# Optimization experiments

Measured on AMD Instinct MI355X. Metric: run time of the kernel, lower is better.

Reference implementation:

```python
import jax, jax.numpy as jnp
import numpy as np

B, N, DIM = 8, 1024, 768
HEADS = 8
NUM_CH = 3
S = 16  # sqrt(DIM // NUM_CH)
HEAD_DIM = DIM // HEADS
BN_EPS = 1e-3  # keras BatchNormalization default epsilon


def setup_inputs() -> dict:
    key = jax.random.key(0)
    ks = jax.random.split(key, 6)
    return {
        "q": jax.random.normal(ks[0], (B, N, DIM), jnp.float32),
        "k": jax.random.normal(ks[1], (B, N, DIM), jnp.float32),
        "v": jax.random.normal(ks[2], (B, N, DIM), jnp.float32),
        # qconv2d kernel (HWIO); source applies qconv2d to q, k AND v (kconv/vconv are dead)
        "conv_w": jax.random.normal(ks[3], (3, 3, NUM_CH, NUM_CH), jnp.float32) * 0.1,
        # re-attention 1x1 conv over the heads channel: (in_heads, out_heads) + bias
        "reatten_w": jax.random.normal(ks[4], (HEADS, HEADS), jnp.float32) * 0.3,
        "reatten_b": jnp.zeros((HEADS,), jnp.float32),
        # BatchNorm (inference) params over the heads channel
        "bn_gamma": jnp.ones((HEADS,), jnp.float32),
        "bn_beta": jnp.zeros((HEADS,), jnp.float32),
        "bn_mean": jnp.zeros((HEADS,), jnp.float32),
        "bn_var": jnp.ones((HEADS,), jnp.float32),
        "proj_w": jax.random.normal(ks[5], (DIM, DIM), jnp.float32) * 0.02,
        "proj_b": jnp.zeros((DIM,), jnp.float32),
    }


def _heads(x, conv_w):
    # x: (B, N, P) -> unflatten to (B*N, S, S, C) images, 3x3 SAME conv, split heads
    b, n, p = x.shape
    img = x.reshape(b * n, S, S, NUM_CH)
    y = jax.lax.conv_general_dilated(
        img, conv_w, window_strides=(1, 1), padding="SAME",
        dimension_numbers=("NHWC", "HWIO", "NHWC"))
    # (B, N, heads, head_dim) -> (B, heads, N, head_dim)
    return y.reshape(b, n, HEADS, p // HEADS).transpose(0, 2, 1, 3)


def reference(q, k, v, conv_w, reatten_w, reatten_b,
              bn_gamma, bn_beta, bn_mean, bn_var, proj_w, proj_b):
    scale = HEAD_DIM ** (-0.5)
    reatten_scale = 1.0  # transform_scale=False
    qh = _heads(q, conv_w)
    kh = _heads(k, conv_w)
    vh = _heads(v, conv_w)
    # (B, heads, N, N) attention map
    attn = jax.nn.softmax(jnp.einsum("bhnd,bhmd->bhnm", qh, kh) * scale, axis=-1)
    # re-attention: 1x1 conv mixing heads + inference BatchNorm over heads channel
    attn = jnp.einsum("bhnm,hg->bgnm", attn, reatten_w) + reatten_b[None, :, None, None]
    inv = bn_gamma * jax.lax.rsqrt(bn_var + BN_EPS)
    attn = (attn - bn_mean[None, :, None, None]) * inv[None, :, None, None] \
           + bn_beta[None, :, None, None]
    attn = attn * reatten_scale
    out = jnp.einsum("bhnm,bhmd->bhnd", attn, vh)  # (B, heads, N, head_dim)
    out = out.transpose(0, 2, 1, 3).reshape(q.shape[0], q.shape[1], DIM)
    return out @ proj_w + proj_b
```

## Files before the change

kernel.cpp:

```cpp
#include <hip/hip_runtime.h>
#include <hip/hip_bf16.h>
#include <stdint.h>

typedef __hip_bfloat16 bf16;
typedef __attribute__((ext_vector_type(8))) short short8;
typedef __attribute__((ext_vector_type(4))) float f32x4;

#define DEVFN __device__ __forceinline__

constexpr float SCALE = 0.10206207261596577f;

DEVFN short8 as_s8(uint4 u) { union { uint4 a; short8 b; } x; x.a = u; return x.b; }

DEVFN f32x4 mfma16(uint4 a, uint4 b, f32x4 c) {
  return __builtin_amdgcn_mfma_f32_16x16x32_bf16(as_s8(a), as_s8(b), c, 0, 0, 0);
}

DEVFN uint4 ldg4(const bf16* p) { return *(const uint4*)p; }

__global__ __launch_bounds__(256) void conv_kernel(
    const float* __restrict__ q, const float* __restrict__ k, const float* __restrict__ v,
    const float* __restrict__ cw,
    bf16* __restrict__ qh, bf16* __restrict__ kh, bf16* __restrict__ vh)
{
  __shared__ float img[3][768];
  __shared__ float wsm[81];
  const int t = threadIdx.x;
  const size_t pos = blockIdx.x;
  const int b = blockIdx.x >> 10;
  const int n = blockIdx.x & 1023;

  {
    const float* s0 = q + pos * 768;
    const float* s1 = k + pos * 768;
    const float* s2 = v + pos * 768;
    img[0][t] = s0[t]; img[0][t + 256] = s0[t + 256]; img[0][t + 512] = s0[t + 512];
    img[1][t] = s1[t]; img[1][t + 256] = s1[t + 256]; img[1][t + 512] = s1[t + 512];
    img[2][t] = s2[t]; img[2][t + 256] = s2[t + 256]; img[2][t + 512] = s2[t + 512];
  }
  if (t < 81) wsm[t] = cw[t];
  __syncthreads();

  const int x    = t & 15;
  const int y    = t >> 4;
  const int head = y >> 1;
  const int d0   = (y & 1) * 48 + x * 3;
  const size_t obase = (((size_t)(b * 8 + head)) * 1024 + n) * 96 + d0;

  #pragma unroll
  for (int s3 = 0; s3 < 3; ++s3) {
    float a0 = 0.f, a1 = 0.f, a2 = 0.f;
    #pragma unroll
    for (int dy = 0; dy < 3; ++dy) {
      const int iy = y + dy - 1;
      if ((unsigned)iy < 16u) {
        #pragma unroll
        for (int dx = 0; dx < 3; ++dx) {
          const int ix = x + dx - 1;
          if ((unsigned)ix < 16u) {
            const int ib = iy * 48 + ix * 3;
            const int wb = (dy * 3 + dx) * 9;
            #pragma unroll
            for (int ci = 0; ci < 3; ++ci) {
              const float val = img[s3][ib + ci];
              a0 = fmaf(val, wsm[wb + ci * 3 + 0], a0);
              a1 = fmaf(val, wsm[wb + ci * 3 + 1], a1);
              a2 = fmaf(val, wsm[wb + ci * 3 + 2], a2);
            }
          }
        }
      }
    }
    bf16* dst = (s3 == 0) ? qh : (s3 == 1) ? kh : vh;
    dst[obase]     = __float2bfloat16(a0);
    dst[obase + 1] = __float2bfloat16(a1);
    dst[obase + 2] = __float2bfloat16(a2);
  }
}

__global__ __launch_bounds__(256) void vtrans_kernel(
    const bf16* __restrict__ vh, bf16* __restrict__ vt)
{
  __shared__ unsigned T[64][52];
  const int t = threadIdx.x;
  const int bg = blockIdx.x >> 4;
  const int n0 = (blockIdx.x & 15) << 6;
  const bf16* src = vh + ((size_t)bg * 1024 + n0) * 96;
  #pragma unroll
  for (int it = 0; it < 3; ++it) {
    const int i = t + it * 256;
    const int r = i / 12, j = i - r * 12;
    ((uint4*)&T[r][0])[j] = ((const uint4*)(src + (size_t)r * 96))[j];
  }
  __syncthreads();
  #pragma unroll
  for (int it = 0; it < 3; ++it) {
    const int i = t + it * 256;
    const int d = i >> 3, c = i & 7;
    unsigned wo[4];
    #pragma unroll
    for (int p = 0; p < 4; ++p) {
      const unsigned lo = T[c * 8 + p * 2    ][d >> 1];
      const unsigned hi = T[c * 8 + p * 2 + 1][d >> 1];
      const unsigned a  = (d & 1) ? (lo >> 16)          : (lo & 0xffffu);
      const unsigned bs = (d & 1) ? (hi & 0xffff0000u)  : (hi << 16);
      wo[p] = a | bs;
    }
    uint4 out4; out4.x = wo[0]; out4.y = wo[1]; out4.z = wo[2]; out4.w = wo[3];
    *(uint4*)(vt + ((size_t)bg * 96 + d) * 1024 + n0 + c * 8) = out4;
  }
}

__global__ __launch_bounds__(512, 2) void attn_fused(
    const bf16* __restrict__ qh, const bf16* __restrict__ kh, const bf16* __restrict__ vt,
    const float* __restrict__ rw, const float* __restrict__ rb,
    const float* __restrict__ bng, const float* __restrict__ bnb,
    const float* __restrict__ bnm, const float* __restrict__ bnv,
    float* __restrict__ X)
{
  __shared__ bf16  Qsm[8][32][104];
  __shared__ bf16  Am[8][32][64];
  __shared__ float Lsm[8][32];
  __shared__ float Linv[8][32];
  __shared__ float Wm[8][8];
  __shared__ float invg[8], cg[8];

  const int t    = threadIdx.x;
  const int b    = blockIdx.x & 7;
  const int nt   = blockIdx.x >> 3;
  const int n0   = nt << 5;
  const int w    = t >> 6;
  const int lane = t & 63;
  const int l15  = lane & 15;
  const int quad = lane >> 4;
  const int nh   = w >> 2;
  const int mq   = w & 3;

  {
    const int row  = t >> 1;
    const int half = t & 1;
    const int hh = row >> 5, nn = row & 31;
    const bf16* src = qh + (((size_t)(b * 8 + hh)) * 1024 + n0 + nn) * 96 + half * 48;
    bf16* dst = &Qsm[hh][nn][half * 48];
    #pragma unroll
    for (int j = 0; j < 6; ++j)
      ((uint4*)dst)[j] = ((const uint4*)src)[j];
  }
  if (t < 64) Wm[t >> 3][t & 7] = rw[t];
  if (t < 8) {
    const float iv = bng[t] * rsqrtf(bnv[t] + 1e-3f);
    invg[t] = iv;
    cg[t]   = iv * (rb[t] - bnm[t]) + bnb[t];
  }
  if (t < 256) Lsm[t >> 5][t & 31] = 0.f;
  __syncthreads();

  const bf16* kbase = kh + (size_t)(b * 8) * 98304;
  const size_t kfragoff = (size_t)(mq * 16 + l15) * 96 + quad * 8;
  const int qrow = nh * 16 + l15;

  uint4 kf[8][3];
  #pragma unroll
  for (int hp = 0; hp < 3; ++hp) {
    const bf16* kp = kbase + (size_t)hp * 98304 + kfragoff;
    kf[hp][0] = ldg4(kp); kf[hp][1] = ldg4(kp + 32); kf[hp][2] = ldg4(kp + 64);
  }

  float lac[8][4];
  #pragma unroll
  for (int h = 0; h < 8; ++h)
    #pragma unroll
    for (int r = 0; r < 4; ++r) lac[h][r] = 0.f;

  #pragma unroll 1
  for (int mt = 0; mt < 16; ++mt) {
    const int m0  = mt << 6;
    const int m0n = (mt < 15) ? m0 + 64 : 0;
    #pragma unroll
    for (int h = 0; h < 8; ++h) {
      {
        const int ht = (h + 3) & 7;
        const bf16* kp = kbase + (size_t)ht * 98304
                       + (size_t)((h < 5) ? m0 : m0n) * 96 + kfragoff;
        uint4 p0 = ldg4(kp), p1 = ldg4(kp + 32), p2 = ldg4(kp + 64);
        const uint4 q0 = *(const uint4*)&Qsm[h][qrow][quad * 8];
        const uint4 q1 = *(const uint4*)&Qsm[h][qrow][32 + quad * 8];
        const uint4 q2 = *(const uint4*)&Qsm[h][qrow][64 + quad * 8];
        f32x4 acc = {0.f, 0.f, 0.f, 0.f};
        acc = mfma16(q0, kf[h][0], acc);
        acc = mfma16(q1, kf[h][1], acc);
        acc = mfma16(q2, kf[h][2], acc);
        kf[ht][0] = p0; kf[ht][1] = p1; kf[ht][2] = p2;
        #pragma unroll
        for (int r = 0; r < 4; ++r)
          lac[h][r] += __expf(fminf(acc[r] * SCALE, 25.f));
      }
    }
  }
  #pragma unroll
  for (int h = 0; h < 8; ++h)
    #pragma unroll
    for (int off = 1; off < 16; off <<= 1)
      #pragma unroll
      for (int r = 0; r < 4; ++r) lac[h][r] += __shfl_xor(lac[h][r], off);
  if (l15 == 0) {
    #pragma unroll
    for (int h = 0; h < 8; ++h)
      #pragma unroll
      for (int r = 0; r < 4; ++r)
        atomicAdd(&Lsm[h][nh * 16 + quad * 4 + r], lac[h][r]);
  }
  __syncthreads();
  if (t < 256) Linv[t >> 5][t & 31] = 1.f / Lsm[t >> 5][t & 31];
  __syncthreads();

  f32x4 oacc[2][6];
  #pragma unroll
  for (int i = 0; i < 2; ++i)
    #pragma unroll
    for (int j = 0; j < 6; ++j) oacc[i][j] = (f32x4){0.f, 0.f, 0.f, 0.f};

  const int nrow = nh * 16 + quad * 4;

  #pragma unroll 1
  for (int mt = 0; mt < 16; ++mt) {
    const int m0  = mt << 6;
    const int m0n = (mt < 15) ? m0 + 64 : 0;

    float aloc[8][4];
    #pragma unroll
    for (int g = 0; g < 8; ++g)
      #pragma unroll
      for (int r = 0; r < 4; ++r) aloc[g][r] = 0.f;

    #pragma unroll
    for (int h = 0; h < 8; ++h) {
      const int ht = (h + 3) & 7;
      const bf16* kp = kbase + (size_t)ht * 98304
                     + (size_t)((h < 5) ? m0 : m0n) * 96 + kfragoff;
      uint4 p0 = ldg4(kp), p1 = ldg4(kp + 32), p2 = ldg4(kp + 64);
      const uint4 q0 = *(const uint4*)&Qsm[h][qrow][quad * 8];
      const uint4 q1 = *(const uint4*)&Qsm[h][qrow][32 + quad * 8];
      const uint4 q2 = *(const uint4*)&Qsm[h][qrow][64 + quad * 8];
      f32x4 acc = {0.f, 0.f, 0.f, 0.f};
      acc = mfma16(q0, kf[h][0], acc);
      acc = mfma16(q1, kf[h][1], acc);
      acc = mfma16(q2, kf[h][2], acc);
      kf[ht][0] = p0; kf[ht][1] = p1; kf[ht][2] = p2;

      const f32x4 li  = *(const f32x4*)&Linv[h][nrow];
      const f32x4 wlo = *(const f32x4*)&Wm[h][0];
      const f32x4 whi = *(const f32x4*)&Wm[h][4];
      float p[4];
      #pragma unroll
      for (int r = 0; r < 4; ++r)
        p[r] = __expf(fminf(acc[r] * SCALE, 25.f)) * li[r];
      #pragma unroll
      for (int g = 0; g < 4; ++g)
        #pragma unroll
        for (int r = 0; r < 4; ++r) {
          aloc[g][r]     = fmaf(p[r], wlo[g], aloc[g][r]);
          aloc[g + 4][r] = fmaf(p[r], whi[g], aloc[g + 4][r]);
        }
    }

    uint4 vf[6][2];
    #pragma unroll
    for (int dt = 0; dt < 6; ++dt) {
      const bf16* vp = vt + (((size_t)(b * 8 + w)) * 96 + dt * 16 + l15) * 1024
                     + m0 + quad * 8;
      vf[dt][0] = ldg4(vp); vf[dt][1] = ldg4(vp + 32);
    }

    #pragma unroll
    for (int g = 0; g < 8; ++g) {
      const float iv = invg[g], cc = cg[g];
      #pragma unroll
      for (int r = 0; r < 4; ++r) {
        const int n = nrow + r;
        const int m = (mq * 16 + l15) ^ ((n & 7) << 3);
        Am[g][n][m] = __float2bfloat16(fmaf(iv, aloc[g][r], cc));
      }
    }
    __syncthreads();

    #pragma unroll
    for (int nn2 = 0; nn2 < 2; ++nn2) {
      const int arow = nn2 * 16 + l15;
      const int sw   = (arow & 7) << 3;
      const uint4 a0 = *(const uint4*)&Am[w][arow][(quad * 8) ^ sw];
      const uint4 a1 = *(const uint4*)&Am[w][arow][(32 + quad * 8) ^ sw];
      #pragma unroll
      for (int dt = 0; dt < 6; ++dt) {
        oacc[nn2][dt] = mfma16(a0, vf[dt][0], oacc[nn2][dt]);
        oacc[nn2][dt] = mfma16(a1, vf[dt][1], oacc[nn2][dt]);
      }
    }
    __syncthreads();
  }

  const size_t xbase = ((size_t)(b * 1024 + n0)) * 768;
  #pragma unroll
  for (int nn2 = 0; nn2 < 2; ++nn2)
    #pragma unroll
    for (int dt = 0; dt < 6; ++dt)
      #pragma unroll
      for (int r = 0; r < 4; ++r)
        X[xbase + (size_t)(nn2 * 16 + quad * 4 + r) * 768 + w * 96 + dt * 16 + l15]
            = oacc[nn2][dt][r];
}

__global__ __launch_bounds__(256) void wsplit_kernel(
    const float* __restrict__ pw, ushort* __restrict__ WhT, ushort* __restrict__ WlT)
{
  __shared__ float T[32][33];
  const int t  = threadIdx.x;
  const int kt = (blockIdx.x % 24) * 32;
  const int nt = (blockIdx.x / 24) * 32;
  #pragma unroll
  for (int it = 0; it < 4; ++it) {
    const int i = t + it * 256;
    const int r = i >> 5, c = i & 31;
    T[r][c] = pw[(size_t)(kt + r) * 768 + nt + c];
  }
  __syncthreads();
  #pragma unroll
  for (int it = 0; it < 4; ++it) {
    const int i = t + it * 256;
    const int r = i >> 5, c = i & 31;
    const float x = T[c][r];
    const float fhi = __bfloat162float(__float2bfloat16(x));
    const float flo = x - fhi;
    WhT[(size_t)(nt + r) * 768 + kt + c] = (ushort)(__float_as_uint(fhi) >> 16);
    WlT[(size_t)(nt + r) * 768 + kt + c] =
        (ushort)(__float_as_uint(__bfloat162float(__float2bfloat16(flo))) >> 16);
  }
}

DEVFN void split2(float f0, float f1, unsigned& hw, unsigned& lw) {
  const float h0 = __bfloat162float(__float2bfloat16(f0));
  const float h1 = __bfloat162float(__float2bfloat16(f1));
  hw = (__float_as_uint(h0) >> 16) | (__float_as_uint(h1) & 0xffff0000u);
  const unsigned l0 = __float_as_uint(__bfloat162float(__float2bfloat16(f0 - h0))) >> 16;
  const unsigned l1 = __float_as_uint(__bfloat162float(__float2bfloat16(f1 - h1))) & 0xffff0000u;
  lw = l0 | l1;
}

__global__ __launch_bounds__(256) void proj3_kernel(
    const float* __restrict__ X,
    const ushort* __restrict__ WhT, const ushort* __restrict__ WlT,
    const float* __restrict__ pb, float* __restrict__ out)
{
  __shared__ unsigned Ah[64][36], Al[64][36], Bh[64][36], Bl[64][36];
  const int t    = threadIdx.x;
  const int bc   = blockIdx.x % 12, br = blockIdx.x / 12;
  const int row0 = br * 64, col0 = bc * 64;
  const int w    = t >> 6;
  const int lane = t & 63;
  const int l15  = lane & 15;
  const int quad = lane >> 4;
  const int wr   = w >> 1, wc = w & 1;

  f32x4 acc[2][2];
  #pragma unroll
  for (int i = 0; i < 2; ++i)
    #pragma unroll
    for (int j = 0; j < 2; ++j) acc[i][j] = (f32x4){0.f, 0.f, 0.f, 0.f};

  for (int kt = 0; kt < 768; kt += 64) {
    __syncthreads();
    #pragma unroll
    for (int it = 0; it < 2; ++it) {
      const int i = t + it * 256;
      const int r = i >> 3, j = i & 7;
      const float* xs = X + (size_t)(row0 + r) * 768 + kt + j * 8;
      const float4 xa = *(const float4*)(xs);
      const float4 xb = *(const float4*)(xs + 4);
      uint4 hv, lv;
      split2(xa.x, xa.y, hv.x, lv.x);
      split2(xa.z, xa.w, hv.y, lv.y);
      split2(xb.x, xb.y, hv.z, lv.z);
      split2(xb.z, xb.w, hv.w, lv.w);
      ((uint4*)&Ah[r][0])[j] = hv;
      ((uint4*)&Al[r][0])[j] = lv;
      ((uint4*)&Bh[r][0])[j] = *(const uint4*)(WhT + (size_t)(col0 + r) * 768 + kt + j * 8);
      ((uint4*)&Bl[r][0])[j] = *(const uint4*)(WlT + (size_t)(col0 + r) * 768 + kt + j * 8);
    }
    __syncthreads();
    #pragma unroll
    for (int ks = 0; ks < 2; ++ks) {
      const int ko = ks * 16 + quad * 4;
      uint4 ah[2], al[2], bh[2], bl[2];
      #pragma unroll
      for (int i = 0; i < 2; ++i) {
        ah[i] = *(const uint4*)&Ah[wr * 32 + i * 16 + l15][ko];
        al[i] = *(const uint4*)&Al[wr * 32 + i * 16 + l15][ko];
      }
      #pragma unroll
      for (int j = 0; j < 2; ++j) {
        bh[j] = *(const uint4*)&Bh[wc * 32 + j * 16 + l15][ko];
        bl[j] = *(const uint4*)&Bl[wc * 32 + j * 16 + l15][ko];
      }
      #pragma unroll
      for (int i = 0; i < 2; ++i)
        #pragma unroll
        for (int j = 0; j < 2; ++j) {
          acc[i][j] = mfma16(ah[i], bh[j], acc[i][j]);
          acc[i][j] = mfma16(al[i], bh[j], acc[i][j]);
          acc[i][j] = mfma16(ah[i], bl[j], acc[i][j]);
        }
    }
  }

  #pragma unroll
  for (int i = 0; i < 2; ++i)
    #pragma unroll
    for (int j = 0; j < 2; ++j) {
      const int col = col0 + wc * 32 + j * 16 + l15;
      const float bias = pb[col];
      #pragma unroll
      for (int r = 0; r < 4; ++r)
        out[(size_t)(row0 + wr * 32 + i * 16 + quad * 4 + r) * 768 + col] = acc[i][j][r] + bias;
    }
}

extern "C" void kernel_launch(void* const* d_in, const int* in_sizes, int n_in,
                              void* d_out, int out_size, void* d_ws, size_t ws_size,
                              hipStream_t stream)
{
  const float* q  = (const float*)d_in[0];
  const float* k  = (const float*)d_in[1];
  const float* v  = (const float*)d_in[2];
  const float* cw = (const float*)d_in[3];
  const float* rw = (const float*)d_in[4];
  const float* rb = (const float*)d_in[5];
  const float* bg = (const float*)d_in[6];
  const float* bb = (const float*)d_in[7];
  const float* bm = (const float*)d_in[8];
  const float* bv = (const float*)d_in[9];
  const float* pw = (const float*)d_in[10];
  const float* pb = (const float*)d_in[11];
  float* out = (float*)d_out;

  char* ws = (char*)d_ws;
  bf16*  qh = (bf16*)(ws);
  bf16*  kh = (bf16*)(ws + 12582912);
  bf16*  vt = (bf16*)(ws + 25165824);
  float* X  = (float*)(ws + 37748736);
  bf16*  vhT = (bf16*)X;
  ushort* WhT = (ushort*)vt;
  ushort* WlT = (ushort*)((char*)vt + 1179648);

  conv_kernel<<<8192, 256, 0, stream>>>(q, k, v, cw, qh, kh, vhT);
  vtrans_kernel<<<1024, 256, 0, stream>>>(vhT, vt);
  attn_fused<<<256, 512, 0, stream>>>(qh, kh, vt, rw, rb, bg, bb, bm, bv, X);
  wsplit_kernel<<<576, 256, 0, stream>>>(pw, WhT, WlT);
  proj3_kernel<<<1536, 256, 0, stream>>>(X, WhT, WlT, pb, out);
}
```

Baseline: 351.1 us.

## Widen key tile to 128 per iteration, each wave covering all 32 query rows

The attention kernel now gives each of the 8 waves a distinct 16-key slice of a 128-wide key tile, and each wave computes both 16-row query halves. Previously the waves split 2 query halves by 4 key quarters over a 64-wide tile. Each K fragment now feeds two MFMAs, halving the key loop trip count and the number of block barriers. The attention-map LDS buffer doubles to 128 columns with a new XOR swizzle, and the V fragment loads are software-pipelined in 32-column chunks between the PV MFMAs. The cost is more registers (doubled lac/aloc accumulators) and more LDS, which may hurt occupancy at the 512x2 launch bounds.

```diff
diff --git a/kernel.cpp b/kernel.cpp
--- a/kernel.cpp
+++ b/kernel.cpp
@@ -17,6 +17,8 @@
 }
 
 DEVFN uint4 ldg4(const bf16* p) { return *(const uint4*)p; }
+
+DEVFN int amsw(int n) { return ((n & 3) << 3) | (((n >> 2) & 3) << 4); }
 
 __global__ __launch_bounds__(256) void conv_kernel(
     const float* __restrict__ q, const float* __restrict__ k, const float* __restrict__ v,
@@ -119,7 +121,7 @@
     float* __restrict__ X)
 {
   __shared__ bf16  Qsm[8][32][104];
-  __shared__ bf16  Am[8][32][64];
+  __shared__ bf16  Am[8][32][128];
   __shared__ float Lsm[8][32];
   __shared__ float Linv[8][32];
   __shared__ float Wm[8][8];
@@ -133,8 +135,6 @@
   const int lane = t & 63;
   const int l15  = lane & 15;
   const int quad = lane >> 4;
-  const int nh   = w >> 2;
-  const int mq   = w & 3;
 
   {
     const int row  = t >> 1;
@@ -156,8 +156,7 @@
   __syncthreads();
 
   const bf16* kbase = kh + (size_t)(b * 8) * 98304;
-  const size_t kfragoff = (size_t)(mq * 16 + l15) * 96 + quad * 8;
-  const int qrow = nh * 16 + l15;
+  const size_t kfragoff = (size_t)(w * 16 + l15) * 96 + quad * 8;
 
   uint4 kf[8][3];
   #pragma unroll
@@ -166,134 +165,189 @@
     kf[hp][0] = ldg4(kp); kf[hp][1] = ldg4(kp + 32); kf[hp][2] = ldg4(kp + 64);
   }
 
-  float lac[8][4];
+  float lac[8][2][4];
   #pragma unroll
   for (int h = 0; h < 8; ++h)
     #pragma unroll
-    for (int r = 0; r < 4; ++r) lac[h][r] = 0.f;
+    for (int nh2 = 0; nh2 < 2; ++nh2)
+      #pragma unroll
+      for (int r = 0; r < 4; ++r) lac[h][nh2][r] = 0.f;
 
   #pragma unroll 1
-  for (int mt = 0; mt < 16; ++mt) {
-    const int m0  = mt << 6;
-    const int m0n = (mt < 15) ? m0 + 64 : 0;
-    #pragma unroll
-    for (int h = 0; h < 8; ++h) {
-      {
-        const int ht = (h + 3) & 7;
-        const bf16* kp = kbase + (size_t)ht * 98304
-                       + (size_t)((h < 5) ? m0 : m0n) * 96 + kfragoff;
-        uint4 p0 = ldg4(kp), p1 = ldg4(kp + 32), p2 = ldg4(kp + 64);
-        const uint4 q0 = *(const uint4*)&Qsm[h][qrow][quad * 8];
-        const uint4 q1 = *(const uint4*)&Qsm[h][qrow][32 + quad * 8];
-        const uint4 q2 = *(const uint4*)&Qsm[h][qrow][64 + quad * 8];
-        f32x4 acc = {0.f, 0.f, 0.f, 0.f};
-        acc = mfma16(q0, kf[h][0], acc);
-        acc = mfma16(q1, kf[h][1], acc);
-        acc = mfma16(q2, kf[h][2], acc);
-        kf[ht][0] = p0; kf[ht][1] = p1; kf[ht][2] = p2;
-        #pragma unroll
-        for (int r = 0; r < 4; ++r)
-          lac[h][r] += __expf(fminf(acc[r] * SCALE, 25.f));
-      }
-    }
-  }
-  #pragma unroll
-  for (int h = 0; h < 8; ++h)
-    #pragma unroll
-    for (int off = 1; off < 16; off <<= 1)
-      #pragma unroll
-      for (int r = 0; r < 4; ++r) lac[h][r] += __shfl_xor(lac[h][r], off);
-  if (l15 == 0) {
-    #pragma unroll
-    for (int h = 0; h < 8; ++h)
-      #pragma unroll
-      for (int r = 0; r < 4; ++r)
-        atomicAdd(&Lsm[h][nh * 16 + quad * 4 + r], lac[h][r]);
-  }
-  __syncthreads();
-  if (t < 256) Linv[t >> 5][t & 31] = 1.f / Lsm[t >> 5][t & 31];
-  __syncthreads();
-
-  f32x4 oacc[2][6];
-  #pragma unroll
-  for (int i = 0; i < 2; ++i)
-    #pragma unroll
-    for (int j = 0; j < 6; ++j) oacc[i][j] = (f32x4){0.f, 0.f, 0.f, 0.f};
-
-  const int nrow = nh * 16 + quad * 4;
-
-  #pragma unroll 1
-  for (int mt = 0; mt < 16; ++mt) {
-    const int m0  = mt << 6;
-    const int m0n = (mt < 15) ? m0 + 64 : 0;
-
-    float aloc[8][4];
-    #pragma unroll
-    for (int g = 0; g < 8; ++g)
-      #pragma unroll
-      for (int r = 0; r < 4; ++r) aloc[g][r] = 0.f;
-
+  for (int mt = 0; mt < 8; ++mt) {
+    const int m0  = mt << 7;
+    const int m0n = (mt < 7) ? m0 + 128 : 0;
     #pragma unroll
     for (int h = 0; h < 8; ++h) {
       const int ht = (h + 3) & 7;
       const bf16* kp = kbase + (size_t)ht * 98304
                      + (size_t)((h < 5) ? m0 : m0n) * 96 + kfragoff;
       uint4 p0 = ldg4(kp), p1 = ldg4(kp + 32), p2 = ldg4(kp + 64);
-      const uint4 q0 = *(const uint4*)&Qsm[h][qrow][quad * 8];
-      const uint4 q1 = *(const uint4*)&Qsm[h][qrow][32 + quad * 8];
-      const uint4 q2 = *(const uint4*)&Qsm[h][qrow][64 + quad * 8];
-      f32x4 acc = {0.f, 0.f, 0.f, 0.f};
-      acc = mfma16(q0, kf[h][0], acc);
-      acc = mfma16(q1, kf[h][1], acc);
-      acc = mfma16(q2, kf[h][2], acc);
+      const uint4 qa0 = *(const uint4*)&Qsm[h][l15][quad * 8];
+      const uint4 qa1 = *(const uint4*)&Qsm[h][l15][32 + quad * 8];
+      const uint4 qa2 = *(const uint4*)&Qsm[h][l15][64 + quad * 8];
+      const uint4 qb0 = *(const uint4*)&Qsm[h][16 + l15][quad * 8];
+      const uint4 qb1 = *(const uint4*)&Qsm[h][16 + l15][32 + quad * 8];
+      const uint4 qb2 = *(const uint4*)&Qsm[h][16 + l15][64 + quad * 8];
+      f32x4 a0 = {0.f, 0.f, 0.f, 0.f}, a1 = {0.f, 0.f, 0.f, 0.f};
+      a0 = mfma16(qa0, kf[h][0], a0);
+      a1 = mfma16(qb0, kf[h][0], a1);
+      a0 = mfma16(qa1, kf[h][1], a0);
+      a1 = mfma16(qb1, kf[h][1], a1);
+      a0 = mfma16(qa2, kf[h][2], a0);
+      a1 = mfma16(qb2, kf[h][2], a1);
       kf[ht][0] = p0; kf[ht][1] = p1; kf[ht][2] = p2;
-
-      const f32x4 li  = *(const f32x4*)&Linv[h][nrow];
+      #pragma unroll
+      for (int r = 0; r < 4; ++r) {
+        lac[h][0][r] += __expf(fminf(a0[r] * SCALE, 25.f));
+        lac[h][1][r] += __expf(fminf(a1[r] * SCALE, 25.f));
+      }
+    }
+  }
+  #pragma unroll
+  for (int h = 0; h < 8; ++h)
+    #pragma unroll
+    for (int nh2 = 0; nh2 < 2; ++nh2)
+      #pragma unroll
+      for (int off = 1; off < 16; off <<= 1)
+        #pragma unroll
+        for (int r = 0; r < 4; ++r)
+          lac[h][nh2][r] += __shfl_xor(lac[h][nh2][r], off);
+  if (l15 == 0) {
+    #pragma unroll
+    for (int h = 0; h < 8; ++h)
+      #pragma unroll
+      for (int nh2 = 0; nh2 < 2; ++nh2)
+        #pragma unroll
+        for (int r = 0; r < 4; ++r)
+          atomicAdd(&Lsm[h][nh2 * 16 + quad * 4 + r], lac[h][nh2][r]);
+  }
+  __syncthreads();
+  if (t < 256) Linv[t >> 5][t & 31] = 1.f / Lsm[t >> 5][t & 31];
+  __syncthreads();
+
+  f32x4 oacc[2][6];
+  #pragma unroll
+  for (int i = 0; i < 2; ++i)
+    #pragma unroll
+    for (int j = 0; j < 6; ++j) oacc[i][j] = (f32x4){0.f, 0.f, 0.f, 0.f};
+
+  const size_t vrow = ((size_t)(b * 8 + w)) * 96 + l15;
+
+  #pragma unroll 1
+  for (int mt = 0; mt < 8; ++mt) {
+    const int m0  = mt << 7;
+    const int m0n = (mt < 7) ? m0 + 128 : 0;
+
+    float aloc[8][2][4];
+    #pragma unroll
+    for (int g = 0; g < 8; ++g)
+      #pragma unroll
+      for (int nh2 = 0; nh2 < 2; ++nh2)
+        #pragma unroll
+        for (int r = 0; r < 4; ++r) aloc[g][nh2][r] = 0.f;
+
+    #pragma unroll
+    for (int h = 0; h < 8; ++h) {
+      const int ht = (h + 3) & 7;
+      const bf16* kp = kbase + (size_t)ht * 98304
+                     + (size_t)((h < 5) ? m0 : m0n) * 96 + kfragoff;
+      uint4 p0 = ldg4(kp), p1 = ldg4(kp + 32), p2 = ldg4(kp + 64);
+      const uint4 qa0 = *(const uint4*)&Qsm[h][l15][quad * 8];
+      const uint4 qa1 = *(const uint4*)&Qsm[h][l15][32 + quad * 8];
+      const uint4 qa2 = *(const uint4*)&Qsm[h][l15][64 + quad * 8];
+      const uint4 qb0 = *(const uint4*)&Qsm[h][16 + l15][quad * 8];
+      const uint4 qb1 = *(const uint4*)&Qsm[h][16 + l15][32 + quad * 8];
+      const uint4 qb2 = *(const uint4*)&Qsm[h][16 + l15][64 + quad * 8];
+      f32x4 a0 = {0.f, 0.f, 0.f, 0.f}, a1 = {0.f, 0.f, 0.f, 0.f};
+      a0 = mfma16(qa0, kf[h][0], a0);
+      a1 = mfma16(qb0, kf[h][0], a1);
+      a0 = mfma16(qa1, kf[h][1], a0);
+      a1 = mfma16(qb1, kf[h][1], a1);
+      a0 = mfma16(qa2, kf[h][2], a0);
+      a1 = mfma16(qb2, kf[h][2], a1);
+      kf[ht][0] = p0; kf[ht][1] = p1; kf[ht][2] = p2;
+
       const f32x4 wlo = *(const f32x4*)&Wm[h][0];
       const f32x4 whi = *(const f32x4*)&Wm[h][4];
-      float p[4];
-      #pragma unroll
-      for (int r = 0; r < 4; ++r)
-        p[r] = __expf(fminf(acc[r] * SCALE, 25.f)) * li[r];
-      #pragma unroll
-      for (int g = 0; g < 4; ++g)
+      #pragma unroll
+      for (int nh2 = 0; nh2 < 2; ++nh2) {
+        const f32x4 li = *(const f32x4*)&Linv[h][nh2 * 16 + quad * 4];
+        float p[4];
         #pragma unroll
         for (int r = 0; r < 4; ++r) {
-          aloc[g][r]     = fmaf(p[r], wlo[g], aloc[g][r]);
-          aloc[g + 4][r] = fmaf(p[r], whi[g], aloc[g + 4][r]);
+          const float s = (nh2 ? a1[r] : a0[r]) * SCALE;
+          p[r] = __expf(fminf(s, 25.f)) * li[r];
         }
-    }
-
-    uint4 vf[6][2];
-    #pragma unroll
-    for (int dt = 0; dt < 6; ++dt) {
-      const bf16* vp = vt + (((size_t)(b * 8 + w)) * 96 + dt * 16 + l15) * 1024
-                     + m0 + quad * 8;
-      vf[dt][0] = ldg4(vp); vf[dt][1] = ldg4(vp + 32);
-    }
+        #pragma unroll
+        for (int g = 0; g < 4; ++g)
+          #pragma unroll
+          for (int r = 0; r < 4; ++r) {
+            aloc[g][nh2][r]     = fmaf(p[r], wlo[g], aloc[g][nh2][r]);
+            aloc[g + 4][nh2][r] = fmaf(p[r], whi[g], aloc[g + 4][nh2][r]);
+          }
+      }
+    }
+
+    uint4 vA[6], vB[6];
+    #pragma unroll
+    for (int dt = 0; dt < 6; ++dt)
+      vA[dt] = ldg4(vt + (vrow + dt * 16) * 1024 + m0 + quad * 8);
 
     #pragma unroll
     for (int g = 0; g < 8; ++g) {
       const float iv = invg[g], cc = cg[g];
       #pragma unroll
-      for (int r = 0; r < 4; ++r) {
-        const int n = nrow + r;
-        const int m = (mq * 16 + l15) ^ ((n & 7) << 3);
-        Am[g][n][m] = __float2bfloat16(fmaf(iv, aloc[g][r], cc));
-      }
+      for (int nh2 = 0; nh2 < 2; ++nh2)
+        #pragma unroll
+        for (int r = 0; r < 4; ++r) {
+          const int n = nh2 * 16 + quad * 4 + r;
+          const int m = (w * 16 + l15) ^ amsw(n);
+          Am[g][n][m] = __float2bfloat16(fmaf(iv, aloc[g][nh2][r], cc));
+        }
     }
     __syncthreads();
 
     #pragma unroll
-    for (int nn2 = 0; nn2 < 2; ++nn2) {
-      const int arow = nn2 * 16 + l15;
-      const int sw   = (arow & 7) << 3;
-      const uint4 a0 = *(const uint4*)&Am[w][arow][(quad * 8) ^ sw];
-      const uint4 a1 = *(const uint4*)&Am[w][arow][(32 + quad * 8) ^ sw];
+    for (int dt = 0; dt < 6; ++dt)
+      vB[dt] = ldg4(vt + (vrow + dt * 16) * 1024 + m0 + 32 + quad * 8);
+
+    {
+      const int arow0 = l15, arow1 = 16 + l15;
+      const int sw0 = amsw(arow0), sw1 = amsw(arow1);
+      uint4 a0 = *(const uint4*)&Am[w][arow0][(quad * 8) ^ sw0];
+      uint4 a1 = *(const uint4*)&Am[w][arow1][(quad * 8) ^ sw1];
       #pragma unroll
       for (int dt = 0; dt < 6; ++dt) {
-        oacc[nn2][dt] = mfma16(a0, vf[dt][0], oacc[nn2][dt]);
-        oacc[nn2][dt] = mfma16(a1, vf[dt][1], oacc[nn2][dt]);
+        oacc[0][dt] = mfma16(a0, vA[dt], oacc[0][dt]);
+        oacc[1][dt] = mfma16(a1, vA[dt], oacc[1][dt]);
+      }
+      #pragma unroll
+      for (int dt = 0; dt < 6; ++dt)
+        vA[dt] = ldg4(vt + (vrow + dt * 16) * 1024 + m0 + 64 + quad * 8);
+      a0 = *(const uint4*)&Am[w][arow0][(32 + quad * 8) ^ sw0];
+      a1 = *(const uint4*)&Am[w][arow1][(32 + quad * 8) ^ sw1];
+      #pragma unroll
+      for (int dt = 0; dt < 6; ++dt) {
+        oacc[0][dt] = mfma16(a0, vB[dt], oacc[0][dt]);
+        oacc[1][dt] = mfma16(a1, vB[dt], oacc[1][dt]);
+      }
+      #pragma unroll
+      for (int dt = 0; dt < 6; ++dt)
+        vB[dt] = ldg4(vt + (vrow + dt * 16) * 1024 + m0 + 96 + quad * 8);
+      a0 = *(const uint4*)&Am[w][arow0][(64 + quad * 8) ^ sw0];
+      a1 = *(const uint4*)&Am[w][arow1][(64 + quad * 8) ^ sw1];
+      #pragma unroll
+      for (int dt = 0; dt < 6; ++dt) {
+        oacc[0][dt] = mfma16(a0, vA[dt], oacc[0][dt]);
+        oacc[1][dt] = mfma16(a1, vA[dt], oacc[1][dt]);
+      }
+      a0 = *(const uint4*)&Am[w][arow0][(96 + quad * 8) ^ sw0];
+      a1 = *(const uint4*)&Am[w][arow1][(96 + quad * 8) ^ sw1];
+      #pragma unroll
+      for (int dt = 0; dt < 6; ++dt) {
+        oacc[0][dt] = mfma16(a0, vB[dt], oacc[0][dt]);
+        oacc[1][dt] = mfma16(a1, vB[dt], oacc[1][dt]);
       }
     }
     __syncthreads();
@@ -301,13 +355,13 @@
 
   const size_t xbase = ((size_t)(b * 1024 + n0)) * 768;
   #pragma unroll
-  for (int nn2 = 0; nn2 < 2; ++nn2)
+  for (int nh2 = 0; nh2 < 2; ++nh2)
     #pragma unroll
     for (int dt = 0; dt < 6; ++dt)
       #pragma unroll
       for (int r = 0; r < 4; ++r)
-        X[xbase + (size_t)(nn2 * 16 + quad * 4 + r) * 768 + w * 96 + dt * 16 + l15]
-            = oacc[nn2][dt][r];
+        X[xbase + (size_t)(nh2 * 16 + quad * 4 + r) * 768 + w * 96 + dt * 16 + l15]
+            = oacc[nh2][dt][r];
 }
 
 __global__ __launch_bounds__(256) void wsplit_kernel(
```

After: 355.6 us. About the same (+1.3%).
